# Kernel tuning notes

Hardware: AMD Instinct MI355X
Metric: run time of the kernel (lower is better)

Reference implementation:

```python
import jax, jax.numpy as jnp
import numpy as np

ENTITY_NUM = 100000
RELATION_NUM = 500
EMB_DIM = 128
BATCH = 8


def setup_inputs() -> dict:
    key = jax.random.key(0)
    k1, k2, k3, k4 = jax.random.split(key, 4)
    return {
        "head": jax.random.randint(k1, (BATCH,), 0, ENTITY_NUM),
        "relation": jax.random.randint(k2, (BATCH,), 0, RELATION_NUM),
        "tail": jnp.arange(ENTITY_NUM),  # test mode: all entities as candidate tails
        "emb_entity": jax.random.normal(k3, (ENTITY_NUM, EMB_DIM), dtype=jnp.float32),
        "emb_relation": jax.random.normal(k4, (RELATION_NUM, EMB_DIM), dtype=jnp.float32),
        "bias_head": jnp.zeros((ENTITY_NUM, 1), dtype=jnp.float32),
        "bias_tail": jnp.zeros((ENTITY_NUM, 1), dtype=jnp.float32),
    }


def reference(head, relation, tail, emb_entity, emb_relation, bias_head, bias_tail):
    # TransE test mode ('test.batch'): score every entity as tail for each query.
    emb_head = emb_entity[head]            # (B, D)
    emb_rel = emb_relation[relation]       # (B, D)
    emb_tail = emb_entity[tail]            # (E, D)
    b_head = bias_head[head]               # (B, 1)
    b_tail = bias_tail[tail]               # (E, 1)

    emb_pred_tail = (emb_head + emb_rel)[:, None, :]      # (B, 1, D)
    all_dev = emb_tail[None, :, :] - emb_pred_tail        # (B, E, D)
    score = jnp.linalg.norm(all_dev, axis=2) + b_head + b_tail.reshape(1, -1)
    return score  # (B, E)
```

## Files before the change

### kernel.cpp

```cpp
#include <hip/hip_runtime.h>

#define BQ  8
#define DIM 128

typedef __attribute__((ext_vector_type(8))) short bf16x8;
typedef __attribute__((ext_vector_type(4))) float f32x4;

__device__ __forceinline__ unsigned pack2(float x, float y) {
    unsigned xb = __float_as_uint(x) + 0x8000u;
    unsigned yb = __float_as_uint(y) + 0x8000u;
    return __builtin_amdgcn_perm(yb, xb, 0x07060302u);
}

__global__ __launch_bounds__(256) void transe_mfma(
    const int*   __restrict__ head,
    const int*   __restrict__ relation,
    const int*   __restrict__ tail,
    const float* __restrict__ emb_entity,
    const float* __restrict__ emb_relation,
    const float* __restrict__ bias_head,
    const float* __restrict__ bias_tail,
    float*       __restrict__ out,
    int E)
{
    __shared__ float pred[BQ][DIM];
    __shared__ float p2_s[BQ];
    __shared__ float bh_s[BQ];

    const int t = threadIdx.x;

    for (int i = t; i < BQ * DIM; i += 256) {
        int b = i >> 7, d = i & 127;
        pred[b][d] = emb_entity[(size_t)head[b] * DIM + d]
                   + emb_relation[(size_t)relation[b] * DIM + d];
    }
    if (t < BQ) bh_s[t] = bias_head[head[t]];
    __syncthreads();
    {
        int q = t >> 5, l5 = t & 31;
        float4 v = *(const float4*)&pred[q][l5 << 2];
        float s = v.x*v.x + v.y*v.y + v.z*v.z + v.w*v.w;
        s += __shfl_xor(s, 1, 32);  s += __shfl_xor(s, 2, 32);
        s += __shfl_xor(s, 4, 32);  s += __shfl_xor(s, 8, 32);
        s += __shfl_xor(s, 16, 32);
        if (l5 == 0) p2_s[q] = s;
    }
    __syncthreads();

    const int lane = t & 63;
    const int wid  = t >> 6;
    const int col  = lane & 15;
    const int g    = lane >> 4;

    bf16x8 B0, B1, B2, B3;
    {
        union { unsigned u[4]; bf16x8 v; } bb;
        #pragma unroll
        for (int mi = 0; mi < 4; ++mi) {
            #pragma unroll
            for (int jp = 0; jp < 4; ++jp) {
                float x = 0.f, y = 0.f;
                if (col < BQ) {
                    const float* pp = &pred[col][mi*32 + g*8 + jp*2];
                    x = -2.f * pp[0];
                    y = -2.f * pp[1];
                }
                bb.u[jp] = pack2(x, y);
            }
            if      (mi == 0) B0 = bb.v;
            else if (mi == 1) B1 = bb.v;
            else if (mi == 2) B2 = bb.v;
            else              B3 = bb.v;
        }
    }
    const float p2c = (col < BQ) ? p2_s[col] : 0.f;
    const float bhc = (col < BQ) ? bh_s[col] : 0.f;

    const int ntiles  = (E + 15) >> 4;
    const int wstride = gridDim.x * 4;
    int tile = blockIdx.x * 4 + wid;
    if (tile >= ntiles) return;

#define STAGE(TL, TE, BT, F0,F1,F2,F3,F4,F5,F6,F7) do {                     \
        int _e = min((TL)*16 + col, E-1);                                   \
        TE = tail[_e];                                                      \
        BT = bias_tail[TE];                                                 \
        const float* _r = emb_entity + (size_t)TE * DIM + g*8;              \
        F0 = *(const float4*)(_r);        F1 = *(const float4*)(_r+4);      \
        F2 = *(const float4*)(_r+32);     F3 = *(const float4*)(_r+36);     \
        F4 = *(const float4*)(_r+64);     F5 = *(const float4*)(_r+68);     \
        F6 = *(const float4*)(_r+96);     F7 = *(const float4*)(_r+100);    \
    } while (0)

#define SSQ4(S, V) S = fmaf(V.x,V.x, fmaf(V.y,V.y, fmaf(V.z,V.z, fmaf(V.w,V.w, S))))

    int teA; float btA; float4 a0,a1,a2,a3,a4,a5,a6,a7;
    STAGE(tile, teA, btA, a0,a1,a2,a3,a4,a5,a6,a7);

    while (true) {
        int  tn   = tile + wstride;
        bool more = (tn < ntiles);
        int teB; float btB; float4 b0,b1,b2,b3,b4,b5,b6,b7;
        if (more) STAGE(tn, teB, btB, b0,b1,b2,b3,b4,b5,b6,b7);

        float ss = 0.f;
        SSQ4(ss, a0); SSQ4(ss, a1); SSQ4(ss, a2); SSQ4(ss, a3);
        SSQ4(ss, a4); SSQ4(ss, a5); SSQ4(ss, a6); SSQ4(ss, a7);
        float t2 = ss + __shfl_xor(ss, 16, 64);
        t2 += __shfl_xor(t2, 32, 64);

        union { unsigned u[4]; bf16x8 v; } A0, A1, A2, A3;
        A0.u[0]=pack2(a0.x,a0.y); A0.u[1]=pack2(a0.z,a0.w);
        A0.u[2]=pack2(a1.x,a1.y); A0.u[3]=pack2(a1.z,a1.w);
        A1.u[0]=pack2(a2.x,a2.y); A1.u[1]=pack2(a2.z,a2.w);
        A1.u[2]=pack2(a3.x,a3.y); A1.u[3]=pack2(a3.z,a3.w);
        A2.u[0]=pack2(a4.x,a4.y); A2.u[1]=pack2(a4.z,a4.w);
        A2.u[2]=pack2(a5.x,a5.y); A2.u[3]=pack2(a5.z,a5.w);
        A3.u[0]=pack2(a6.x,a6.y); A3.u[1]=pack2(a6.z,a6.w);
        A3.u[2]=pack2(a7.x,a7.y); A3.u[3]=pack2(a7.z,a7.w);

        f32x4 C = {0.f, 0.f, 0.f, 0.f};
        C = __builtin_amdgcn_mfma_f32_16x16x32_bf16(A0.v, B0, C, 0, 0, 0);
        C = __builtin_amdgcn_mfma_f32_16x16x32_bf16(A1.v, B1, C, 0, 0, 0);
        C = __builtin_amdgcn_mfma_f32_16x16x32_bf16(A2.v, B2, C, 0, 0, 0);
        C = __builtin_amdgcn_mfma_f32_16x16x32_bf16(A3.v, B3, C, 0, 0, 0);

        int rb = g * 4;
        float t20 = __shfl(t2, rb+0, 64), bt0 = __shfl(btA, rb+0, 64);
        float t21 = __shfl(t2, rb+1, 64), bt1 = __shfl(btA, rb+1, 64);
        float t22 = __shfl(t2, rb+2, 64), bt2 = __shfl(btA, rb+2, 64);
        float t23 = __shfl(t2, rb+3, 64), bt3 = __shfl(btA, rb+3, 64);
        float r0 = sqrtf(fmaxf(C[0] + t20 + p2c, 0.f)) + bhc + bt0;
        float r1 = sqrtf(fmaxf(C[1] + t21 + p2c, 0.f)) + bhc + bt1;
        float r2 = sqrtf(fmaxf(C[2] + t22 + p2c, 0.f)) + bhc + bt2;
        float r3 = sqrtf(fmaxf(C[3] + t23 + p2c, 0.f)) + bhc + bt3;

        if (col < BQ) {
            int e0 = tile * 16 + rb;
            if (e0 + 4 <= E) {
                float4 r; r.x = r0; r.y = r1; r.z = r2; r.w = r3;
                *(float4*)&out[(size_t)col * E + e0] = r;
            } else {
                if (e0 + 0 < E) out[(size_t)col*E + e0 + 0] = r0;
                if (e0 + 1 < E) out[(size_t)col*E + e0 + 1] = r1;
                if (e0 + 2 < E) out[(size_t)col*E + e0 + 2] = r2;
                if (e0 + 3 < E) out[(size_t)col*E + e0 + 3] = r3;
            }
        }

        if (!more) break;
        tile = tn; teA = teB; btA = btB;
        a0=b0; a1=b1; a2=b2; a3=b3; a4=b4; a5=b5; a6=b6; a7=b7;
    }
#undef STAGE
#undef SSQ4
}

extern "C" void kernel_launch(void* const* d_in, const int* in_sizes, int n_in,
                              void* d_out, int out_size, void* d_ws, size_t ws_size,
                              hipStream_t stream) {
    const int*   head         = (const int*)  d_in[0];
    const int*   relation     = (const int*)  d_in[1];
    const int*   tail         = (const int*)  d_in[2];
    const float* emb_entity   = (const float*)d_in[3];
    const float* emb_relation = (const float*)d_in[4];
    const float* bias_head    = (const float*)d_in[5];
    const float* bias_tail    = (const float*)d_in[6];
    float* out = (float*)d_out;

    const int E = in_sizes[2];
    const int ntiles = (E + 15) >> 4;

    int blocks = 1024;
    int maxb = (ntiles + 3) / 4;
    if (blocks > maxb) blocks = maxb;

    hipLaunchKernelGGL(transe_mfma, dim3(blocks), dim3(256), 0, stream,
                       head, relation, tail, emb_entity, emb_relation,
                       bias_head, bias_tail, out, E);
}
```

Measured before the change: 19.47 us.

## Replace grid-stride loop with one tile per wave and early gather

Drops the persistent grid-stride loop with software prefetch. The kernel now launches one wave per 16-entity tile (about 1563 blocks) and issues the tail-index and embedding-row loads before the shared-memory prologue, so they overlap with building pred. This exposes more parallelism and hides the global-load latency behind the prologue. In exchange, every block recomputes the pred and norm prologue and the B-operand packing, which adds redundant work and extra launches of short blocks.

```diff
diff --git a/kernel.cpp b/kernel.cpp
--- a/kernel.cpp
+++ b/kernel.cpp
@@ -27,7 +27,19 @@
     __shared__ float p2_s[BQ];
     __shared__ float bh_s[BQ];
 
-    const int t = threadIdx.x;
+    const int t    = threadIdx.x;
+    const int lane = t & 63;
+    const int wid  = t >> 6;
+    const int col  = lane & 15;
+    const int g    = lane >> 4;
+
+    const int ntiles = (E + 15) >> 4;
+    const int tile   = blockIdx.x * 4 + wid;
+    const bool live  = (tile < ntiles);
+
+    int e0 = tile * 16;
+    int te = 0;
+    if (live) te = tail[min(e0 + col, E - 1)];
 
     for (int i = t; i < BQ * DIM; i += 256) {
         int b = i >> 7, d = i & 127;
@@ -35,7 +47,20 @@
                    + emb_relation[(size_t)relation[b] * DIM + d];
     }
     if (t < BQ) bh_s[t] = bias_head[head[t]];
+
+    float bt = 0.f;
+    float4 a0, a1, a2, a3, a4, a5, a6, a7;
+    a0=a1=a2=a3=a4=a5=a6=a7 = make_float4(0.f,0.f,0.f,0.f);
+    if (live) {
+        bt = bias_tail[te];
+        const float* r = emb_entity + (size_t)te * DIM + g * 8;
+        a0 = *(const float4*)(r);       a1 = *(const float4*)(r + 4);
+        a2 = *(const float4*)(r + 32);  a3 = *(const float4*)(r + 36);
+        a4 = *(const float4*)(r + 64);  a5 = *(const float4*)(r + 68);
+        a6 = *(const float4*)(r + 96);  a7 = *(const float4*)(r + 100);
+    }
     __syncthreads();
+
     {
         int q = t >> 5, l5 = t & 31;
         float4 v = *(const float4*)&pred[q][l5 << 2];
@@ -47,10 +72,7 @@
     }
     __syncthreads();
 
-    const int lane = t & 63;
-    const int wid  = t >> 6;
-    const int col  = lane & 15;
-    const int g    = lane >> 4;
+    if (!live) return;
 
     bf16x8 B0, B1, B2, B3;
     {
@@ -76,84 +98,52 @@
     const float p2c = (col < BQ) ? p2_s[col] : 0.f;
     const float bhc = (col < BQ) ? bh_s[col] : 0.f;
 
-    const int ntiles  = (E + 15) >> 4;
-    const int wstride = gridDim.x * 4;
-    int tile = blockIdx.x * 4 + wid;
-    if (tile >= ntiles) return;
+#define SSQ4(S, V) S = fmaf(V.x,V.x, fmaf(V.y,V.y, fmaf(V.z,V.z, fmaf(V.w,V.w, S))))
+    float ss = 0.f;
+    SSQ4(ss, a0); SSQ4(ss, a1); SSQ4(ss, a2); SSQ4(ss, a3);
+    SSQ4(ss, a4); SSQ4(ss, a5); SSQ4(ss, a6); SSQ4(ss, a7);
+    float t2 = ss + __shfl_xor(ss, 16, 64);
+    t2 += __shfl_xor(t2, 32, 64);
+#undef SSQ4
 
-#define STAGE(TL, TE, BT, F0,F1,F2,F3,F4,F5,F6,F7) do {                     \
-        int _e = min((TL)*16 + col, E-1);                                   \
-        TE = tail[_e];                                                      \
-        BT = bias_tail[TE];                                                 \
-        const float* _r = emb_entity + (size_t)TE * DIM + g*8;              \
-        F0 = *(const float4*)(_r);        F1 = *(const float4*)(_r+4);      \
-        F2 = *(const float4*)(_r+32);     F3 = *(const float4*)(_r+36);     \
-        F4 = *(const float4*)(_r+64);     F5 = *(const float4*)(_r+68);     \
-        F6 = *(const float4*)(_r+96);     F7 = *(const float4*)(_r+100);    \
-    } while (0)
+    union { unsigned u[4]; bf16x8 v; } A0, A1, A2, A3;
+    A0.u[0]=pack2(a0.x,a0.y); A0.u[1]=pack2(a0.z,a0.w);
+    A0.u[2]=pack2(a1.x,a1.y); A0.u[3]=pack2(a1.z,a1.w);
+    A1.u[0]=pack2(a2.x,a2.y); A1.u[1]=pack2(a2.z,a2.w);
+    A1.u[2]=pack2(a3.x,a3.y); A1.u[3]=pack2(a3.z,a3.w);
+    A2.u[0]=pack2(a4.x,a4.y); A2.u[1]=pack2(a4.z,a4.w);
+    A2.u[2]=pack2(a5.x,a5.y); A2.u[3]=pack2(a5.z,a5.w);
+    A3.u[0]=pack2(a6.x,a6.y); A3.u[1]=pack2(a6.z,a6.w);
+    A3.u[2]=pack2(a7.x,a7.y); A3.u[3]=pack2(a7.z,a7.w);
 
-#define SSQ4(S, V) S = fmaf(V.x,V.x, fmaf(V.y,V.y, fmaf(V.z,V.z, fmaf(V.w,V.w, S))))
+    f32x4 C = {0.f, 0.f, 0.f, 0.f};
+    C = __builtin_amdgcn_mfma_f32_16x16x32_bf16(A0.v, B0, C, 0, 0, 0);
+    C = __builtin_amdgcn_mfma_f32_16x16x32_bf16(A1.v, B1, C, 0, 0, 0);
+    C = __builtin_amdgcn_mfma_f32_16x16x32_bf16(A2.v, B2, C, 0, 0, 0);
+    C = __builtin_amdgcn_mfma_f32_16x16x32_bf16(A3.v, B3, C, 0, 0, 0);
 
-    int teA; float btA; float4 a0,a1,a2,a3,a4,a5,a6,a7;
-    STAGE(tile, teA, btA, a0,a1,a2,a3,a4,a5,a6,a7);
+    int rb = g * 4;
+    float t20 = __shfl(t2, rb+0, 64), bt0 = __shfl(bt, rb+0, 64);
+    float t21 = __shfl(t2, rb+1, 64), bt1 = __shfl(bt, rb+1, 64);
+    float t22 = __shfl(t2, rb+2, 64), bt2 = __shfl(bt, rb+2, 64);
+    float t23 = __shfl(t2, rb+3, 64), bt3 = __shfl(bt, rb+3, 64);
+    float r0 = sqrtf(fmaxf(C[0] + t20 + p2c, 0.f)) + bhc + bt0;
+    float r1 = sqrtf(fmaxf(C[1] + t21 + p2c, 0.f)) + bhc + bt1;
+    float r2 = sqrtf(fmaxf(C[2] + t22 + p2c, 0.f)) + bhc + bt2;
+    float r3 = sqrtf(fmaxf(C[3] + t23 + p2c, 0.f)) + bhc + bt3;
 
-    while (true) {
-        int  tn   = tile + wstride;
-        bool more = (tn < ntiles);
-        int teB; float btB; float4 b0,b1,b2,b3,b4,b5,b6,b7;
-        if (more) STAGE(tn, teB, btB, b0,b1,b2,b3,b4,b5,b6,b7);
-
-        float ss = 0.f;
-        SSQ4(ss, a0); SSQ4(ss, a1); SSQ4(ss, a2); SSQ4(ss, a3);
-        SSQ4(ss, a4); SSQ4(ss, a5); SSQ4(ss, a6); SSQ4(ss, a7);
-        float t2 = ss + __shfl_xor(ss, 16, 64);
-        t2 += __shfl_xor(t2, 32, 64);
-
-        union { unsigned u[4]; bf16x8 v; } A0, A1, A2, A3;
-        A0.u[0]=pack2(a0.x,a0.y); A0.u[1]=pack2(a0.z,a0.w);
-        A0.u[2]=pack2(a1.x,a1.y); A0.u[3]=pack2(a1.z,a1.w);
-        A1.u[0]=pack2(a2.x,a2.y); A1.u[1]=pack2(a2.z,a2.w);
-        A1.u[2]=pack2(a3.x,a3.y); A1.u[3]=pack2(a3.z,a3.w);
-        A2.u[0]=pack2(a4.x,a4.y); A2.u[1]=pack2(a4.z,a4.w);
-        A2.u[2]=pack2(a5.x,a5.y); A2.u[3]=pack2(a5.z,a5.w);
-        A3.u[0]=pack2(a6.x,a6.y); A3.u[1]=pack2(a6.z,a6.w);
-        A3.u[2]=pack2(a7.x,a7.y); A3.u[3]=pack2(a7.z,a7.w);
-
-        f32x4 C = {0.f, 0.f, 0.f, 0.f};
-        C = __builtin_amdgcn_mfma_f32_16x16x32_bf16(A0.v, B0, C, 0, 0, 0);
-        C = __builtin_amdgcn_mfma_f32_16x16x32_bf16(A1.v, B1, C, 0, 0, 0);
-        C = __builtin_amdgcn_mfma_f32_16x16x32_bf16(A2.v, B2, C, 0, 0, 0);
-        C = __builtin_amdgcn_mfma_f32_16x16x32_bf16(A3.v, B3, C, 0, 0, 0);
-
-        int rb = g * 4;
-        float t20 = __shfl(t2, rb+0, 64), bt0 = __shfl(btA, rb+0, 64);
-        float t21 = __shfl(t2, rb+1, 64), bt1 = __shfl(btA, rb+1, 64);
-        float t22 = __shfl(t2, rb+2, 64), bt2 = __shfl(btA, rb+2, 64);
-        float t23 = __shfl(t2, rb+3, 64), bt3 = __shfl(btA, rb+3, 64);
-        float r0 = sqrtf(fmaxf(C[0] + t20 + p2c, 0.f)) + bhc + bt0;
-        float r1 = sqrtf(fmaxf(C[1] + t21 + p2c, 0.f)) + bhc + bt1;
-        float r2 = sqrtf(fmaxf(C[2] + t22 + p2c, 0.f)) + bhc + bt2;
-        float r3 = sqrtf(fmaxf(C[3] + t23 + p2c, 0.f)) + bhc + bt3;
-
-        if (col < BQ) {
-            int e0 = tile * 16 + rb;
-            if (e0 + 4 <= E) {
-                float4 r; r.x = r0; r.y = r1; r.z = r2; r.w = r3;
-                *(float4*)&out[(size_t)col * E + e0] = r;
-            } else {
-                if (e0 + 0 < E) out[(size_t)col*E + e0 + 0] = r0;
-                if (e0 + 1 < E) out[(size_t)col*E + e0 + 1] = r1;
-                if (e0 + 2 < E) out[(size_t)col*E + e0 + 2] = r2;
-                if (e0 + 3 < E) out[(size_t)col*E + e0 + 3] = r3;
-            }
+    if (col < BQ) {
+        int e = e0 + rb;
+        if (e + 4 <= E) {
+            float4 r; r.x = r0; r.y = r1; r.z = r2; r.w = r3;
+            *(float4*)&out[(size_t)col * E + e] = r;
+        } else {
+            if (e + 0 < E) out[(size_t)col*E + e + 0] = r0;
+            if (e + 1 < E) out[(size_t)col*E + e + 1] = r1;
+            if (e + 2 < E) out[(size_t)col*E + e + 2] = r2;
+            if (e + 3 < E) out[(size_t)col*E + e + 3] = r3;
         }
-
-        if (!more) break;
-        tile = tn; teA = teB; btA = btB;
-        a0=b0; a1=b1; a2=b2; a3=b3; a4=b4; a5=b5; a6=b6; a7=b7;
     }
-#undef STAGE
-#undef SSQ4
 }
 
 extern "C" void kernel_launch(void* const* d_in, const int* in_sizes, int n_in,
@@ -170,10 +160,7 @@
 
     const int E = in_sizes[2];
     const int ntiles = (E + 15) >> 4;
-
-    int blocks = 1024;
-    int maxb = (ntiles + 3) / 4;
-    if (blocks > maxb) blocks = maxb;
+    const int blocks = (ntiles + 3) / 4;
 
     hipLaunchKernelGGL(transe_mfma, dim3(blocks), dim3(256), 0, stream,
                        head, relation, tail, emb_entity, emb_relation,
```

Result: faster. 17.91 us (-8.0%).
